# Optimization experiments

Measured on AMD Instinct MI355X. Metric: run time of the kernel, lower is better.

## Reference

```python
import jax, jax.numpy as jnp
import numpy as np

L = 8        # num_layers
REPEAT = 2   # repeats per layer
DIM = 256    # mixer hidden dim
DIM2 = 128   # head dim (divisible by 32 for AvgPool1d(32))
B = 8192
EPS = 1e-5


def hardswish(x):
    return x * jnp.clip(x + 3.0, 0.0, 6.0) * (1.0 / 6.0)


def layernorm(x, g, b):
    m = jnp.mean(x, axis=-1, keepdims=True)
    xc = x - m
    v = jnp.mean(xc * xc, axis=-1, keepdims=True)
    return xc * jax.lax.rsqrt(v + EPS) * g + b


def setup_inputs() -> dict:
    key = jax.random.key(0)
    ks = jax.random.split(key, 32)
    s = 0.1
    inp = {
        "x": jax.random.normal(ks[0], (B, 3, 32, 32), dtype=jnp.float32),
        "conv_w": jax.random.normal(ks[1], (3,), dtype=jnp.float32) * s,
        "conv_b": jax.random.normal(ks[2], (1,), dtype=jnp.float32) * s,
        "fc0_w": jax.random.normal(ks[3], (32, 32), dtype=jnp.float32) * s,
        "fc0_b": jax.random.normal(ks[4], (32,), dtype=jnp.float32) * s,
        "ln1_g": jnp.ones((L, 32), dtype=jnp.float32),
        "ln1_b": jnp.zeros((L, 32), dtype=jnp.float32),
        "w11": jax.random.normal(ks[5], (L, DIM, 32), dtype=jnp.float32) * s,
        "b11": jax.random.normal(ks[6], (L, DIM), dtype=jnp.float32) * s,
        "w12": jax.random.normal(ks[7], (L, 32, DIM), dtype=jnp.float32) * s,
        "b12": jax.random.normal(ks[8], (L, 32), dtype=jnp.float32) * s,
        "ln2_g": jnp.ones((L, 32), dtype=jnp.float32),
        "ln2_b": jnp.zeros((L, 32), dtype=jnp.float32),
        "w21": jax.random.normal(ks[9], (L, DIM, 32), dtype=jnp.float32) * s,
        "b21": jax.random.normal(ks[10], (L, DIM), dtype=jnp.float32) * s,
        "w22": jax.random.normal(ks[11], (L, 32, DIM), dtype=jnp.float32) * s,
        "b22": jax.random.normal(ks[12], (L, 32), dtype=jnp.float32) * s,
        "fc1_w": jax.random.normal(ks[13], (DIM2, 32), dtype=jnp.float32) * s,
        "fc1_b": jax.random.normal(ks[14], (DIM2,), dtype=jnp.float32) * s,
        "fcout_w": jax.random.normal(ks[15], (10, DIM2), dtype=jnp.float32) * s,
        "fcout_b": jax.random.normal(ks[16], (10,), dtype=jnp.float32) * s,
    }
    return inp


def reference(x, conv_w, conv_b, fc0_w, fc0_b, ln1_g, ln1_b, w11, b11, w12, b12,
              ln2_g, ln2_b, w21, b21, w22, b22, fc1_w, fc1_b, fcout_w, fcout_b):
    # rgb_conv: 1x1 conv 3->1 channels, then squeeze -> [B, 32, 32]
    h = jnp.einsum('bchw,c->bhw', x, conv_w) + conv_b[0]
    h = h @ fc0_w.T + fc0_b  # fc0 over last dim (32)

    for i in range(L):
        for _ in range(REPEAT):
            # token-mixing branch (operates along dim 1 via permute)
            t = layernorm(h, ln1_g[i], ln1_b[i])
            t = jnp.swapaxes(t, 1, 2)                      # [B, 32, 32]
            t = hardswish(t @ w11[i].T + b11[i])           # [B, 32, DIM]
            t = t @ w12[i].T + b12[i]                      # [B, 32, 32]
            h = h + jnp.swapaxes(t, 1, 2)
            # channel-mixing branch
            c = layernorm(h, ln2_g[i], ln2_b[i])
            c = hardswish(c @ w21[i].T + b21[i])           # [B, 32, DIM]
            h = h + (c @ w22[i].T + b22[i])                # [B, 32, 32]

    y = hardswish(h @ fc1_w.T + fc1_b)                     # [B, 32, DIM2]
    # AvgPool1d(kernel=32, stride=32) over last dim -> [B, 32, DIM2//32]
    y = y.reshape(y.shape[0], 32, DIM2 // 32, 32).mean(axis=-1)
    y = y.reshape(y.shape[0], -1)                          # [B, DIM2]
    return y @ fcout_w.T + fcout_b                         # [B, 10]
```

## Files before the change

kernel.cpp:

```cpp
#include <hip/hip_runtime.h>

#define LNUM 8

typedef __attribute__((ext_vector_type(4))) float f32x4;
typedef __attribute__((ext_vector_type(2))) float f32x2;
typedef __attribute__((ext_vector_type(8))) _Float16 f16x8;
typedef __attribute__((ext_vector_type(2))) _Float16 f16x2;

#define MFMAH(A,B,C) __builtin_amdgcn_mfma_f32_16x16x32_f16(A,B,C,0,0,0)
#define PKRTZ(a,b) __builtin_bit_cast(f16x2, __builtin_amdgcn_cvt_pkrtz(a,b))

__device__ __forceinline__ float hswish_clamp(float t) {
  return __builtin_amdgcn_fmed3f(t + 3.f, 0.f, 6.f);
}
__device__ __forceinline__ f16x2 hsw_pk(f16x2 t) {
  const f16x2 c3 = {(_Float16)3.0f, (_Float16)3.0f};
  const f16x2 c0 = {(_Float16)0.0f, (_Float16)0.0f};
  const f16x2 c6 = {(_Float16)6.0f, (_Float16)6.0f};
  f16x2 u = t + c3;
  u = __builtin_elementwise_min(__builtin_elementwise_max(u, c0), c6);
  return t * u;
}

__device__ __forceinline__ int hws(int row, int c) {
  return (row << 5) + ((((c >> 2) ^ (row & 7)) << 2) | (c & 3));
}

__global__ void prep_weights(const float* __restrict__ w11, const float* __restrict__ b11,
                             const float* __restrict__ w12, const float* __restrict__ b12,
                             const float* __restrict__ g1,  const float* __restrict__ be1,
                             const float* __restrict__ w21, const float* __restrict__ b21,
                             const float* __restrict__ w22, const float* __restrict__ b22,
                             const float* __restrict__ g2,  const float* __restrict__ be2,
                             const float* __restrict__ fc1w, const float* __restrict__ fc1b,
                             char* __restrict__ ws)
{
  const int lb = blockIdx.x;
  const int t = threadIdx.x;
  if (lb == 16) {
    char* o = ws + (size_t)16 * 34816;
    _Float16* wf = (_Float16*)o;
    float* pr = (float*)(o + 8192);
    #pragma unroll
    for (int i = 0; i < 2; ++i) {
      int s = t + i*256;
      int lane = s & 63;
      int row = (s >> 6)*16 + (lane & 15);
      int kb  = ((lane >> 4) & 3) * 8;
      const float* src = fc1w + row*32 + kb;
      #pragma unroll
      for (int j = 0; j < 8; ++j) wf[s*8 + j] = (_Float16)src[j];
    }
    if (t < 128) pr[t] = fc1b[t];
    return;
  }
  const int lay = lb >> 1, br = lb & 1;
  const float* w1  = (br ? w21 : w11) + lay*8192;
  const float* w2  = (br ? w22 : w12) + lay*8192;
  const float* bb1 = (br ? b21 : b11) + lay*256;
  const float* bb2 = (br ? b22 : b12) + lay*32;
  const float* gg  = (br ? g2  : g1 ) + lay*32;
  const float* bb  = (br ? be2 : be1) + lay*32;
  char* o = ws + (size_t)lb * 34816;
  _Float16* w1f = (_Float16*)o;
  _Float16* w2f = (_Float16*)(o + 16384);
  float* pr  = (float*)(o + 32768);
  #pragma unroll
  for (int i = 0; i < 4; ++i) {
    int s = t + i*256;
    int lane = s & 63;
    int row = (s >> 6)*16 + (lane & 15);
    int kb  = ((lane >> 4) & 3) * 8;
    const float* src = w1 + row*32 + kb;
    #pragma unroll
    for (int j = 0; j < 8; ++j) w1f[s*8 + j] = (_Float16)src[j];
  }
  #pragma unroll
  for (int i = 0; i < 4; ++i) {
    int s = t + i*256;
    int lane = s & 63;
    int tt = s >> 7;
    int nt = (s >> 6) & 1;
    int n  = nt*16 + (lane & 15);
    int qq = (lane >> 4) & 3;
    const float* src = w2 + n*256 + tt*32 + qq*4;
    _Float16* dst = w2f + s*8;
    #pragma unroll
    for (int j = 0; j < 4; ++j) dst[j]     = (_Float16)(src[j]      * (1.0f/6.0f));
    #pragma unroll
    for (int j = 0; j < 4; ++j) dst[4 + j] = (_Float16)(src[16 + j] * (1.0f/6.0f));
  }
  pr[t] = bb1[t];
  if (t < 32)      pr[256 + t] = bb2[t];
  else if (t < 64) pr[256 + t] = gg[t - 32];
  else if (t < 96) pr[256 + t] = bb[t - 64];
}

__global__ __launch_bounds__(256) __attribute__((amdgpu_waves_per_eu(3, 8)))
void mixer_mfma(const float* __restrict__ x,
                const float* __restrict__ conv_w, const float* __restrict__ conv_b,
                const float* __restrict__ fc0_w,  const float* __restrict__ fc0_b,
                const char*  __restrict__ ws,
                const float* __restrict__ fcout_w, const float* __restrict__ fcout_b,
                float* __restrict__ out)
{
  __shared__ float smem[4 * 2176];
  const int tid = threadIdx.x;
  const int wv  = tid >> 6;
  const int lid = tid & 63;
  const int ml  = lid & 15;
  const int q   = lid >> 4;
  const int q4  = q << 2, q8 = q << 3;
  const int sl  = lid >> 5, r = lid & 31;
  const int r7  = r & 7;

  float* hW  = smem + wv * 2176;
  float* stW = hW + 2048;

  const size_t b0 = (size_t)blockIdx.x * 8 + (size_t)wv * 2;

  {
    const size_t b = b0 + sl;
    const float* xb = x + b*3072 + r*32;
    const float cw0 = conv_w[0], cw1 = conv_w[1], cw2 = conv_w[2], cb = conv_b[0];
    float g[32];
    #pragma unroll
    for (int j4 = 0; j4 < 8; ++j4) {
      f32x4 a0 = *(const f32x4*)(xb + j4*4);
      f32x4 a1 = *(const f32x4*)(xb + 1024 + j4*4);
      f32x4 a2 = *(const f32x4*)(xb + 2048 + j4*4);
      #pragma unroll
      for (int e = 0; e < 4; ++e)
        g[j4*4+e] = cw0*a0[e] + cw1*a1[e] + cw2*a2[e] + cb;
    }
    f32x4* hp = (f32x4*)(hW + sl*1024 + (r << 5));
    #pragma unroll
    for (int a = 0; a < 8; ++a) {
      f32x4 w;
      #pragma unroll
      for (int e = 0; e < 4; ++e) {
        const int j = a*4 + e;
        const float* wr = fc0_w + j*32;
        float acc = fc0_b[j];
        #pragma unroll
        for (int k = 0; k < 32; ++k) acc += g[k]*wr[k];
        w[e] = acc;
      }
      hp[a ^ r7] = w;
    }
  }

  for (int lay = 0; lay < LNUM; ++lay)
  for (int rep = 0; rep < 2; ++rep)
  for (int br = 0; br < 2; ++br) {
    const char* wsb = ws + (size_t)(lay*2 + br) * 34816;
    const f16x8* w1f = (const f16x8*)wsb;
    const f16x8* w2f = (const f16x8*)(wsb + 16384);
    const float* pb1 = (const float*)(wsb + 32768);
    const float* pb2 = pb1 + 256;
    const float* pg  = pb1 + 288;
    const float* pbt = pb1 + 320;

    {
      const f32x4* hp = (const f32x4*)(hW + sl*1024 + (r << 5));
      float sum = 0.f, sq = 0.f;
      #pragma unroll
      for (int a = 0; a < 8; ++a) {
        f32x4 v = hp[a ^ r7];
        #pragma unroll
        for (int e = 0; e < 4; ++e) { sum += v[e]; sq += v[e]*v[e]; }
      }
      float m = sum * (1.f/32.f);
      float rstd = rsqrtf(sq*(1.f/32.f) - m*m + 1e-5f);
      *(f32x2*)(stW + ((sl << 5) + r)*2) = (f32x2){m, rstd};
    }

    f16x8 b1[4];
    if (br == 0) {
      const float ga = pg[ml],  gb = pg[16 + ml];
      const float ba = pbt[ml], bb2v = pbt[16 + ml];
      #pragma unroll
      for (int i = 0; i < 8; ++i) {
        const int k = q8 + i;
        f32x2 s0 = *(const f32x2*)(stW + k*2);
        f32x2 s1 = *(const f32x2*)(stW + 64 + k*2);
        #pragma unroll
        for (int mt = 0; mt < 4; ++mt) {
          const int samp = mt >> 1;
          const int c = ((mt & 1) << 4) + ml;
          f32x2 st = samp ? s1 : s0;
          float v = hW[samp*1024 + hws(k, c)];
          float g_ = (mt & 1) ? gb : ga;
          float be = (mt & 1) ? bb2v : ba;
          b1[mt][i] = (_Float16)((v - st[0]) * st[1] * g_ + be);
        }
      }
    } else {
      f32x4 g0 = *(const f32x4*)(pg + q8);
      f32x4 g1 = *(const f32x4*)(pg + q8 + 4);
      f32x4 t0 = *(const f32x4*)(pbt + q8);
      f32x4 t1 = *(const f32x4*)(pbt + q8 + 4);
      #pragma unroll
      for (int mt = 0; mt < 4; ++mt) {
        const int samp = mt >> 1;
        const int row = ((mt & 1) << 4) + ml;
        f32x2 st = *(const f32x2*)(stW + ((samp << 5) + row)*2);
        const f32x4* hr = (const f32x4*)(hW + samp*1024 + (row << 5));
        f32x4 v0 = hr[(2*q)     ^ (row & 7)];
        f32x4 v1 = hr[(2*q + 1) ^ (row & 7)];
        #pragma unroll
        for (int e = 0; e < 4; ++e) {
          b1[mt][e]     = (_Float16)((v0[e] - st[0]) * st[1] * g0[e] + t0[e]);
          b1[mt][4 + e] = (_Float16)((v1[e] - st[0]) * st[1] * g1[e] + t1[e]);
        }
      }
    }

    f32x4 acc2[2][4];
    if (br == 0) {
      const float i0 = pb2[ml], i1 = pb2[16 + ml];
      #pragma unroll
      for (int mt = 0; mt < 4; ++mt) {
        acc2[0][mt] = (f32x4){i0, i0, i0, i0};
        acc2[1][mt] = (f32x4){i1, i1, i1, i1};
      }
    } else {
      f32x4 i0 = *(const f32x4*)(pb2 + q4);
      f32x4 i1 = *(const f32x4*)(pb2 + 16 + q4);
      #pragma unroll
      for (int mt = 0; mt < 4; ++mt) { acc2[0][mt] = i0; acc2[1][mt] = i1; }
    }
    #pragma unroll 2
    for (int t = 0; t < 8; ++t) {
      f16x8 a1a = w1f[(t*2 + 0)*64 + lid];
      f16x8 a1b = w1f[(t*2 + 1)*64 + lid];
      f32x4 biasa = *(const f32x4*)(pb1 + t*32 + q4);
      f32x4 biasb = *(const f32x4*)(pb1 + t*32 + 16 + q4);
      f16x8 a2a = w2f[(t*2 + 0)*64 + lid];
      f16x8 a2b = w2f[(t*2 + 1)*64 + lid];
      #pragma unroll
      for (int mt = 0; mt < 4; ++mt) {
        f32x4 c1a = MFMAH(a1a, b1[mt], biasa);
        f32x4 c1b = MFMAH(a1b, b1[mt], biasb);
        union { f16x2 h2[4]; f16x8 v; } b2u;
        b2u.h2[0] = hsw_pk(PKRTZ(c1a[0], c1a[1]));
        b2u.h2[1] = hsw_pk(PKRTZ(c1a[2], c1a[3]));
        b2u.h2[2] = hsw_pk(PKRTZ(c1b[0], c1b[1]));
        b2u.h2[3] = hsw_pk(PKRTZ(c1b[2], c1b[3]));
        if (br == 0) {
          acc2[0][mt] = MFMAH(b2u.v, a2a, acc2[0][mt]);
          acc2[1][mt] = MFMAH(b2u.v, a2b, acc2[1][mt]);
        } else {
          acc2[0][mt] = MFMAH(a2a, b2u.v, acc2[0][mt]);
          acc2[1][mt] = MFMAH(a2b, b2u.v, acc2[1][mt]);
        }
      }
    }

    if (br == 0) {
      #pragma unroll
      for (int mt = 0; mt < 4; ++mt) {
        const int samp = mt >> 1;
        #pragma unroll
        for (int nt = 0; nt < 2; ++nt) {
          const int row = (nt << 4) + ml;
          f32x4* hr = (f32x4*)(hW + samp*1024 + (row << 5));
          const int a = (((mt & 1) << 2) + q) ^ (row & 7);
          f32x4 v = hr[a];
          v += acc2[nt][mt];
          hr[a] = v;
        }
      }
    } else {
      #pragma unroll
      for (int mt = 0; mt < 4; ++mt) {
        const int samp = mt >> 1;
        const int row = ((mt & 1) << 4) + ml;
        f32x4* hr = (f32x4*)(hW + samp*1024 + (row << 5));
        #pragma unroll
        for (int nt = 0; nt < 2; ++nt) {
          const int a = ((nt << 2) + q) ^ (row & 7);
          f32x4 v = hr[a];
          v += acc2[nt][mt];
          hr[a] = v;
        }
      }
    }
  }

  {
    const f16x8* fc1f = (const f16x8*)(ws + (size_t)16 * 34816);
    const float* fb   = (const float*)(ws + (size_t)16 * 34816 + 8192);
    f16x8 be[4];
    #pragma unroll
    for (int mt = 0; mt < 4; ++mt) {
      const int samp = mt >> 1;
      const int row = ((mt & 1) << 4) + ml;
      const f32x4* hr = (const f32x4*)(hW + samp*1024 + (row << 5));
      f32x4 v0 = hr[(2*q)     ^ (row & 7)];
      f32x4 v1 = hr[(2*q + 1) ^ (row & 7)];
      #pragma unroll
      for (int e = 0; e < 4; ++e) {
        be[mt][e]     = (_Float16)v0[e];
        be[mt][4 + e] = (_Float16)v1[e];
      }
    }
    float pl[4][4] = {};
    #pragma unroll
    for (int dt = 0; dt < 8; ++dt) {
      f16x8 af = fc1f[dt*64 + lid];
      f32x4 bias4 = *(const f32x4*)(fb + dt*16 + q4);
      #pragma unroll
      for (int mt = 0; mt < 4; ++mt) {
        f32x4 c = MFMAH(af, be[mt], bias4);
        float s = 0.f;
        #pragma unroll
        for (int rg = 0; rg < 4; ++rg) s += c[rg] * hswish_clamp(c[rg]);
        pl[dt >> 1][mt] += s;
      }
    }
    #pragma unroll
    for (int t = 0; t < 4; ++t)
    #pragma unroll
    for (int mt = 0; mt < 4; ++mt) {
      float v = pl[t][mt];
      v += __shfl_xor(v, 16);
      v += __shfl_xor(v, 32);
      pl[t][mt] = v;
    }
    if (q == 0) {
      #pragma unroll
      for (int mt = 0; mt < 4; ++mt)
      #pragma unroll
      for (int t = 0; t < 4; ++t)
        hW[(mt >> 1)*1024 + (((mt & 1) << 4) + ml)*4 + t] = pl[t][mt];
    }
    if (r < 10) {
      const float* pv = hW + sl*1024;
      const float* wr = fcout_w + r*128;
      float acc = 0.f;
      #pragma unroll
      for (int m4 = 0; m4 < 32; ++m4) {
        f32x4 p4 = *(const f32x4*)(pv + m4*4);
        f32x4 w4 = *(const f32x4*)(wr + m4*4);
        acc += p4[0]*w4[0] + p4[1]*w4[1] + p4[2]*w4[2] + p4[3]*w4[3];
      }
      out[(b0 + sl)*10 + r] = fcout_b[r] + acc * (1.f/192.f);
    }
  }
}

extern "C" void kernel_launch(void* const* d_in, const int* in_sizes, int n_in,
                              void* d_out, int out_size, void* d_ws, size_t ws_size,
                              hipStream_t stream) {
  (void)in_sizes; (void)n_in; (void)out_size; (void)ws_size;
  const float* x       = (const float*)d_in[0];
  const float* conv_w  = (const float*)d_in[1];
  const float* conv_b  = (const float*)d_in[2];
  const float* fc0_w   = (const float*)d_in[3];
  const float* fc0_b   = (const float*)d_in[4];
  const float* ln1_g   = (const float*)d_in[5];
  const float* ln1_b   = (const float*)d_in[6];
  const float* w11     = (const float*)d_in[7];
  const float* b11     = (const float*)d_in[8];
  const float* w12     = (const float*)d_in[9];
  const float* b12     = (const float*)d_in[10];
  const float* ln2_g   = (const float*)d_in[11];
  const float* ln2_b   = (const float*)d_in[12];
  const float* w21     = (const float*)d_in[13];
  const float* b21     = (const float*)d_in[14];
  const float* w22     = (const float*)d_in[15];
  const float* b22     = (const float*)d_in[16];
  const float* fc1_w   = (const float*)d_in[17];
  const float* fc1_b   = (const float*)d_in[18];
  const float* fcout_w = (const float*)d_in[19];
  const float* fcout_b = (const float*)d_in[20];
  float* out = (float*)d_out;
  char* ws = (char*)d_ws;

  prep_weights<<<17, 256, 0, stream>>>(w11, b11, w12, b12, ln1_g, ln1_b,
                                       w21, b21, w22, b22, ln2_g, ln2_b,
                                       fc1_w, fc1_b, ws);
  mixer_mfma<<<1024, 256, 0, stream>>>(x, conv_w, conv_b, fc0_w, fc0_b,
                                       (const char*)ws, fcout_w, fcout_b, out);
}
```

Baseline: 475.5 us.

## Stage per-branch weights in double-buffered LDS with 512-thread blocks

Blocks grow to 512 threads covering 16 samples, and the fp16 MFMA weights for each layer/branch stage are copied cooperatively into a double-buffered LDS region. The next stage's weights are prefetched into registers during compute and written to the other buffer before a block barrier. This replaces per-wave global/L2 weight reads with shared LDS reads. The cost is a __syncthreads per stage, about 132 KB of dynamic LDS per block, and extra registers, which can limit occupancy.

```diff
diff --git a/kernel.cpp b/kernel.cpp
--- a/kernel.cpp
+++ b/kernel.cpp
@@ -96,7 +96,7 @@
   else if (t < 96) pr[256 + t] = bb[t - 64];
 }
 
-__global__ __launch_bounds__(256) __attribute__((amdgpu_waves_per_eu(3, 8)))
+__global__ __launch_bounds__(512, 2)
 void mixer_mfma(const float* __restrict__ x,
                 const float* __restrict__ conv_w, const float* __restrict__ conv_b,
                 const float* __restrict__ fc0_w,  const float* __restrict__ fc0_b,
@@ -104,7 +104,7 @@
                 const float* __restrict__ fcout_w, const float* __restrict__ fcout_b,
                 float* __restrict__ out)
 {
-  __shared__ float smem[4 * 2176];
+  extern __shared__ float smem[];
   const int tid = threadIdx.x;
   const int wv  = tid >> 6;
   const int lid = tid & 63;
@@ -116,8 +116,16 @@
 
   float* hW  = smem + wv * 2176;
   float* stW = hW + 2048;
-
-  const size_t b0 = (size_t)blockIdx.x * 8 + (size_t)wv * 2;
+  char*  wlds = (char*)(smem + 8 * 2176);
+
+  const size_t b0 = (size_t)blockIdx.x * 16 + (size_t)wv * 2;
+
+  f32x4 stg[4];
+  {
+    const f32x4* src = (const f32x4*)ws;
+    #pragma unroll
+    for (int i = 0; i < 4; ++i) stg[i] = src[tid + i*512];
+  }
 
   {
     const size_t b = b0 + sl;
@@ -149,13 +157,27 @@
       hp[a ^ r7] = w;
     }
   }
-
-  for (int lay = 0; lay < LNUM; ++lay)
-  for (int rep = 0; rep < 2; ++rep)
-  for (int br = 0; br < 2; ++br) {
-    const char* wsb = ws + (size_t)(lay*2 + br) * 34816;
-    const f16x8* w1f = (const f16x8*)wsb;
-    const f16x8* w2f = (const f16x8*)(wsb + 16384);
+  {
+    f32x4* dst = (f32x4*)wlds;
+    #pragma unroll
+    for (int i = 0; i < 4; ++i) dst[tid + i*512] = stg[i];
+  }
+  __syncthreads();
+
+  for (int s = 0; s < 32; ++s) {
+    const int cur = s & 1;
+    const int br  = s & 1;
+    const char* wsb = ws + (size_t)(((s >> 2) << 1) + br) * 34816;
+
+    if (s < 31) {
+      const int nreg = (((s + 1) >> 2) << 1) + ((s + 1) & 1);
+      const f32x4* src = (const f32x4*)(ws + (size_t)nreg * 34816);
+      #pragma unroll
+      for (int i = 0; i < 4; ++i) stg[i] = src[tid + i*512];
+    }
+
+    const f16x8* w1f = (const f16x8*)(wlds + cur*32768);
+    const f16x8* w2f = (const f16x8*)(wlds + cur*32768 + 16384);
     const float* pb1 = (const float*)(wsb + 32768);
     const float* pb2 = pb1 + 256;
     const float* pg  = pb1 + 288;
@@ -286,6 +308,13 @@
         }
       }
     }
+
+    if (s < 31) {
+      f32x4* dst = (f32x4*)(wlds + (cur ^ 1)*32768);
+      #pragma unroll
+      for (int i = 0; i < 4; ++i) dst[tid + i*512] = stg[i];
+    }
+    __syncthreads();
   }
 
   {
@@ -378,9 +407,12 @@
   float* out = (float*)d_out;
   char* ws = (char*)d_ws;
 
+  (void)hipFuncSetAttribute(reinterpret_cast<const void*>(mixer_mfma),
+                            hipFuncAttributeMaxDynamicSharedMemorySize, 135168);
+
   prep_weights<<<17, 256, 0, stream>>>(w11, b11, w12, b12, ln1_g, ln1_b,
                                        w21, b21, w22, b22, ln2_g, ln2_b,
                                        fc1_w, fc1_b, ws);
-  mixer_mfma<<<1024, 256, 0, stream>>>(x, conv_w, conv_b, fc0_w, fc0_b,
-                                       (const char*)ws, fcout_w, fcout_b, out);
-}
+  mixer_mfma<<<512, 512, 135168, stream>>>(x, conv_w, conv_b, fc0_w, fc0_b,
+                                           (const char*)ws, fcout_w, fcout_b, out);
+}
```

Measured after the change: 483.1 us. Within noise of the previous version (+1.6%).
